# Performance work log

Hardware: AMD Instinct MI355X
Metric: run time of the kernel (lower is better)

Reference implementation:

```python
import jax, jax.numpy as jnp
import numpy as np
from jax import lax

# ---- static config (from BasePllay_2 / AdTopoLayer(out_features=50, T=25, m0=0.2, lims=[[224,0],[0,224]], K_max=2, p=0)) ----
H = W = 28
G = H * W
T = 25
K_MAX = 2
M0 = 0.2
OUT_FEATURES = 50
B = 32
TSEQ = jnp.linspace(0.0, 100.0, T)  # fixed landscape sample grid (covers DTM value range)

# static grid geometry from lims=[[224,0],[0,224]]
_xs = np.linspace(224.0, 0.0, H)
_ys = np.linspace(0.0, 224.0, W)
_pts = np.stack(np.meshgrid(_xs, _ys, indexing="ij"), -1).reshape(G, 2)
_d = np.sqrt(((_pts[:, None] - _pts[None]) ** 2).sum(-1))
_sidx = np.argsort(_d, axis=-1)
SDIST = jnp.asarray(np.take_along_axis(_d, _sidx, -1), jnp.float32)  # [G,G] sorted distances per grid point
SIDX = jnp.asarray(_sidx.astype(np.int32))                            # [G,G] static distance-sort order

# 4-connectivity neighbor table for the cubical (pixel) grid, -1 = invalid
_ii = np.arange(G).reshape(H, W)
_nb = np.full((H, W, 4), -1, np.int32)
_nb[1:, :, 0] = _ii[:-1, :]
_nb[:-1, :, 1] = _ii[1:, :]
_nb[:, 1:, 2] = _ii[:, :-1]
_nb[:, :-1, 3] = _ii[:, 1:]
NBR = jnp.asarray(_nb.reshape(G, 4))


def dtm(w):
    """Weighted distance-to-measure (r=2) on the fixed grid. w: [B,G] nonneg -> [B,G]."""
    sw = w[:, SIDX]                               # [B,G,G] weights in distance order
    cw = jnp.cumsum(sw, -1)
    d2 = SDIST ** 2
    cwd = jnp.cumsum(sw * d2[None], -1)
    bound = M0 * w.sum(-1)                        # [B]
    k = jnp.argmax(cw >= bound[:, None, None], -1)  # [B,G] first index reaching mass bound
    km1 = jnp.maximum(k - 1, 0)
    take = lambda a, i: jnp.take_along_axis(a, i[..., None], -1)[..., 0]
    has_prev = k > 0
    cw_p = jnp.where(has_prev, take(cw, km1), 0.0)
    cwd_p = jnp.where(has_prev, take(cwd, km1), 0.0)
    dk2 = d2[jnp.arange(G)[None, :], k]           # [B,G]
    val = (cwd_p + (bound[:, None] - cw_p) * dk2) / bound[:, None]
    return jnp.sqrt(jnp.maximum(val, 0.0))


def pd0(vals):
    """0-dim sublevel-set persistence of vals on the pixel grid (union-find, elder rule).
    Returns (births[G], deaths[G]); non-merging pixels yield zero-persistence pairs,
    essential components die at the max filtration value."""
    order = jnp.argsort(vals).astype(jnp.int32)
    rank = jnp.zeros(G, jnp.int32).at[order].set(jnp.arange(G, dtype=jnp.int32))

    def find(parent, i):
        return lax.while_loop(lambda j: parent[j] != j, lambda j: parent[j], i)

    def step(s, carry):
        parent, death = carry
        p = order[s]
        best = p
        for t in range(4):  # unrolled over the 4 grid neighbors (static)
            q = NBR[p, t]
            ok = (q >= 0) & (rank[jnp.maximum(q, 0)] < s)  # neighbor already inserted
            r = find(parent, jnp.where(ok, q, p))
            merge = ok & (r != best)
            r_old = rank[r] < rank[best]
            older = jnp.where(r_old, r, best)
            younger = jnp.where(r_old, best, r)
            widx = jnp.where(merge, younger, G)   # slot G is a dummy
            parent = parent.at[widx].set(older)
            death = death.at[widx].set(p)         # younger component dies at pixel p
            best = jnp.where(merge, older, best)
        return parent, death

    parent0 = jnp.arange(G + 1, dtype=jnp.int32)
    death0 = jnp.full(G + 1, -1, jnp.int32)
    _, death = lax.fori_loop(0, G, step, (parent0, death0))
    d = death[:G]
    deaths = jnp.where(d >= 0, vals[jnp.maximum(d, 0)], vals.max())
    return vals, deaths


def landscape(births, deaths):
    """K_MAX persistence landscapes sampled at TSEQ. [B,G] -> [B, K_MAX*T]."""
    tb = TSEQ[None, :, None] - births[:, None, :]   # [B,T,G]
    td = deaths[:, None, :] - TSEQ[None, :, None]
    tent = jnp.maximum(jnp.minimum(tb, td), 0.0)
    topk = lax.top_k(tent, K_MAX)[0]                # [B,T,K]
    return jnp.transpose(topk, (0, 2, 1)).reshape(births.shape[0], K_MAX * T)


def _forward(x, w_land, b_land, w_fc, b_fc):
    w = x.reshape(x.shape[0], -1)          # nn.Flatten: pixel intensities as measure weights
    v = dtm(w)                             # [B,G]
    births, deaths = jax.vmap(pd0)(v)
    feats = landscape(births, deaths)      # [B, 50]
    xt = feats @ w_land.T + b_land         # AdTopoLayer output [B, out_features]
    signal = jnp.abs(lax.stop_gradient(xt)).sum(0)   # torch: x.detach().abs().sum(0)
    out = jnp.maximum(xt, 0.0) @ w_fc.T + b_fc       # fc(relu(x))
    return out, signal

_forward_jit = jax.jit(_forward)


def setup_inputs() -> dict:
    key = jax.random.key(0)
    k = jax.random.split(key, 4)
    x = jax.random.uniform(k[0], (B, 1, H, W), jnp.float32)  # image-like nonneg weights
    w_land = jax.random.normal(k[1], (OUT_FEATURES, K_MAX * T), jnp.float32) * 0.1
    b_land = jnp.zeros((OUT_FEATURES,), jnp.float32)
    w_fc = jax.random.normal(k[2], (10, OUT_FEATURES), jnp.float32) * 0.1
    b_fc = jnp.zeros((10,), jnp.float32)
    return {"x": x, "w_land": w_land, "b_land": b_land, "w_fc": w_fc, "b_fc": b_fc}


def reference(x, w_land, b_land, w_fc, b_fc):
    return _forward_jit(x, w_land, b_land, w_fc, b_fc)
```

## Files before the change

kernel.cpp:

```cpp
#include <hip/hip_runtime.h>
#include <math.h>

#define H28 28
#define G784 784
#define BATCH 32
#define NOFF 3025
#define NOFFP 3072
#define NKEY 1459
#define TPTS 25
#define KMAX 2
#define NFEAT 50
#define OUTF 50
#define NCLS 10

#define NBX 16
#define BT 512

__device__ __forceinline__ float wave_iscan_f32(float x) {
  int t;
  t = __builtin_amdgcn_update_dpp(0, __float_as_int(x), 0x111, 0xf, 0xf, true);
  x += __int_as_float(t);
  t = __builtin_amdgcn_update_dpp(0, __float_as_int(x), 0x112, 0xf, 0xf, true);
  x += __int_as_float(t);
  t = __builtin_amdgcn_update_dpp(0, __float_as_int(x), 0x114, 0xf, 0xf, true);
  x += __int_as_float(t);
  t = __builtin_amdgcn_update_dpp(0, __float_as_int(x), 0x118, 0xf, 0xf, true);
  x += __int_as_float(t);
  t = __builtin_amdgcn_update_dpp(0, __float_as_int(x), 0x142, 0xa, 0xf, true);
  x += __int_as_float(t);
  t = __builtin_amdgcn_update_dpp(0, __float_as_int(x), 0x143, 0xc, 0xf, true);
  x += __int_as_float(t);
  return x;
}

__global__ __launch_bounds__(BT) void dtm_kernel(const float* __restrict__ x,
                                                 float* __restrict__ v) {
  __shared__ int   hist[NKEY];
  __shared__ int   seg[BT];
  __shared__ unsigned int ofs_ij[NOFFP];
  __shared__ float ofs_d2[NOFFP];
  __shared__ float w_s[G784];
  __shared__ float red[BT];

  const int tid = threadIdx.x;
  const int b   = blockIdx.x;
  const int bx  = blockIdx.y;

  for (int i = tid; i < NKEY; i += BT) hist[i] = 0;
  for (int i = NOFF + tid; i < NOFFP; i += BT) {
    ofs_ij[i] = 0x00640064u;
    ofs_d2[i] = 0.f;
  }
  __syncthreads();
  for (int i = tid; i < NOFF; i += BT) {
    int di = i / 55 - 27, dj = i % 55 - 27;
    atomicAdd(&hist[di * di + dj * dj], 1);
  }
  __syncthreads();

  const int SEG = 3;
  int base0 = tid * SEG;
  int s = 0;
  for (int k = 0; k < SEG; k++) { int idx = base0 + k; if (idx < NKEY) s += hist[idx]; }
  seg[tid] = s;
  __syncthreads();
  for (int off = 1; off < BT; off <<= 1) {
    int add = (tid >= off) ? seg[tid - off] : 0;
    __syncthreads();
    seg[tid] += add;
    __syncthreads();
  }
  int run = seg[tid] - s;
  for (int k = 0; k < SEG; k++) {
    int idx = base0 + k;
    if (idx < NKEY) { int h = hist[idx]; hist[idx] = run; run += h; }
  }
  __syncthreads();

  for (int i = tid; i < NOFF; i += BT) {
    int di = i / 55 - 27, dj = i % 55 - 27;
    int key = di * di + dj * dj;
    int pos = atomicAdd(&hist[key], 1);
    ofs_ij[pos] = ((unsigned)(di & 0xffff)) | (((unsigned)(dj & 0xffff)) << 16);
    float sd = (float)(sqrt((double)key) * (224.0 / 27.0));
    ofs_d2[pos] = sd * sd;
  }

  float ps = 0.f;
  for (int i = tid; i < G784; i += BT) {
    float wv = x[b * G784 + i];
    w_s[i] = wv;
    ps += wv;
  }
  red[tid] = ps;
  __syncthreads();
  for (int off = BT / 2; off > 0; off >>= 1) {
    if (tid < off) red[tid] += red[tid + off];
    __syncthreads();
  }
  const float bound = 0.2f * red[0];

  const int wave = tid >> 6;
  const int lane = tid & 63;
  const int slot = bx * 8 + wave;

  for (int g = slot; g < G784; g += NBX * 8) {
    const int i1 = g / H28, j1 = g % H28;
    float cw = 0.f, cwd = 0.f;
    float cwp = 0.f, cwdp = 0.f, dk2 = 0.f;
    bool crossed = false;
    for (int base = 0; base < NOFFP && !crossed; base += 64) {
      const int o = base + lane;
      const unsigned ij = ofs_ij[o];
      const float d2 = ofs_d2[o];
      const int di = (short)(ij & 0xffffu);
      const int dj = (short)(ij >> 16);
      const int i2 = i1 + di, j2 = j1 + dj;
      const bool inb = ((unsigned)i2 < (unsigned)H28) & ((unsigned)j2 < (unsigned)H28);
      const float wv = inb ? w_s[i2 * H28 + j2] : 0.f;
      const float wd = wv * d2;
      const float psw = wave_iscan_f32(wv);
      const float psd = wave_iscan_f32(wd);
      const unsigned long long mask = __ballot(cw + psw >= bound);
      if (mask) {
        const int f = __ffsll((unsigned long long)mask) - 1;
        const float psw_f = __shfl(psw, f);
        const float w_f   = __shfl(wv, f);
        const float psd_f = __shfl(psd, f);
        const float wd_f  = __shfl(wd, f);
        dk2  = __shfl(d2, f);
        cwp  = cw + (psw_f - w_f);
        cwdp = cwd + (psd_f - wd_f);
        crossed = true;
      } else {
        cw  += __int_as_float(__builtin_amdgcn_readlane(__float_as_int(psw), 63));
        cwd += __int_as_float(__builtin_amdgcn_readlane(__float_as_int(psd), 63));
      }
    }
    const float val = (cwdp + (bound - cwp) * dk2) / bound;
    if (lane == 0) v[b * G784 + g] = sqrtf(fmaxf(val, 0.f));
  }
}

__device__ __forceinline__ unsigned long long pix_key(const float* val_s, int p) {
  return (((unsigned long long)__float_as_uint(val_s[p])) << 10) | (unsigned)p;
}

__global__ __launch_bounds__(256) void pd0_kernel(const float* __restrict__ v,
                                                  float* __restrict__ feats) {
  __shared__ float val_s[G784];
  __shared__ int   ptr_s[G784];
  __shared__ int   parent[G784];
  __shared__ float deathv[G784];
  __shared__ int   mlist[G784];
  __shared__ unsigned long long edges[2048];
  __shared__ float redf[256];
  __shared__ int   mcnt_sh, ecnt_sh;
  __shared__ float vmax_sh;

  const int tid = threadIdx.x;
  const int b   = blockIdx.x;
  if (tid == 0) { mcnt_sh = 0; ecnt_sh = 0; }

  float pm = -1e30f;
  for (int i = tid; i < G784; i += 256) {
    float xv = v[b * G784 + i];
    val_s[i] = xv;
    pm = fmaxf(pm, xv);
  }
  redf[tid] = pm;
  __syncthreads();
  for (int off = 128; off > 0; off >>= 1) {
    if (tid < off) redf[tid] = fmaxf(redf[tid], redf[tid + off]);
    __syncthreads();
  }
  if (tid == 0) vmax_sh = redf[0];
  __syncthreads();
  const float vmax = vmax_sh;

  for (int p = tid; p < G784; p += 256) {
    unsigned long long kp = pix_key(val_s, p);
    int i = p / H28, j = p % H28;
    int nbs[4];
    nbs[0] = (i > 0)       ? p - H28 : -1;
    nbs[1] = (i < H28 - 1) ? p + H28 : -1;
    nbs[2] = (j > 0)       ? p - 1   : -1;
    nbs[3] = (j < H28 - 1) ? p + 1   : -1;
    int best = p;
    unsigned long long bk = kp;
    for (int t = 0; t < 4; t++) {
      int q = nbs[t];
      if (q >= 0) {
        unsigned long long kq = pix_key(val_s, q);
        if (kq < bk) { bk = kq; best = q; }
      }
    }
    ptr_s[p]  = best;
    parent[p] = p;
    deathv[p] = vmax;
    if (best == p) {
      int mi = atomicAdd(&mcnt_sh, 1);
      mlist[mi] = p;
    }
  }
  __syncthreads();

  for (int r = 0; r < 10; r++) {
    for (int p = tid; p < G784; p += 256) ptr_s[p] = ptr_s[ptr_s[p]];
    __syncthreads();
  }

  for (int p = tid; p < G784; p += 256) {
    unsigned long long kp = pix_key(val_s, p);
    int i = p / H28, j = p % H28;
    int nbs[4];
    nbs[0] = (i > 0)       ? p - H28 : -1;
    nbs[1] = (i < H28 - 1) ? p + H28 : -1;
    nbs[2] = (j > 0)       ? p - 1   : -1;
    nbs[3] = (j < H28 - 1) ? p + 1   : -1;
    int bp = ptr_s[p];
    for (int t = 0; t < 4; t++) {
      int q = nbs[t];
      if (q >= 0) {
        unsigned long long kq = pix_key(val_s, q);
        int bq = ptr_s[q];
        if (kq < kp && bq != bp) {
          int e = atomicAdd(&ecnt_sh, 1);
          edges[e] = (((unsigned long long)__float_as_uint(val_s[p])) << 32) |
                     (((unsigned long long)(unsigned)p) << 22) |
                     (((unsigned long long)(unsigned)t) << 20) |
                     (((unsigned long long)(unsigned)bp) << 10) |
                     ((unsigned long long)(unsigned)bq);
        }
      }
    }
  }
  __syncthreads();
  const int ecnt = ecnt_sh;
  const int mcnt = mcnt_sh;

  int n2 = 2;
  while (n2 < ecnt) n2 <<= 1;
  for (int i = ecnt + tid; i < n2; i += 256) edges[i] = ~0ULL;
  __syncthreads();
  for (int kk = 2; kk <= n2; kk <<= 1) {
    for (int jj = kk >> 1; jj > 0; jj >>= 1) {
      for (int i = tid; i < n2; i += 256) {
        int ixj = i ^ jj;
        if (ixj > i) {
          unsigned long long a = edges[i], c = edges[ixj];
          bool up = ((i & kk) == 0);
          if ((a > c) == up) { edges[i] = c; edges[ixj] = a; }
        }
      }
      __syncthreads();
    }
  }

  if (tid < 64) {
    const int target = mcnt - 1;
    int merged = 0;
    for (int base = 0; base < ecnt && merged < target; base += 64) {
      int i = base + tid;
      bool valid = (i < ecnt);
      unsigned long long e = valid ? edges[i] : 0ULL;
      int A = (int)((e >> 10) & 1023u);
      int B = (int)(e & 1023u);
      int rA = valid ? A : 0;
      int rB = valid ? B : 0;
      for (;;) { int pa = parent[rA]; bool mv = (pa != rA); rA = pa; if (!__any(mv)) break; }
      for (;;) { int pb = parent[rB]; bool mv = (pb != rB); rB = pb; if (!__any(mv)) break; }
      unsigned long long mask = __ballot(valid && (rA != rB));
      while (mask && merged < target) {
        int j = __ffsll(mask) - 1;
        mask &= mask - 1;
        unsigned long long ej = edges[base + j];
        int Aj = (int)((ej >> 10) & 1023u);
        int Bj = (int)(ej & 1023u);
        int ra = Aj; for (;;) { int pa = parent[ra]; if (pa == ra) break; ra = pa; }
        int rb = Bj; for (;;) { int pb = parent[rb]; if (pb == rb) break; rb = pb; }
        if (ra != rb) {
          unsigned long long ka = pix_key(val_s, ra);
          unsigned long long kb = pix_key(val_s, rb);
          int older   = (ka < kb) ? ra : rb;
          int younger = (ka < kb) ? rb : ra;
          parent[younger] = older;
          deathv[younger] = __uint_as_float((unsigned)(ej >> 32));
          merged++;
        }
      }
    }
  }
  __syncthreads();

  if (tid < TPTS) {
    float ti = (float)((double)tid * (100.0 / 24.0));
    float t1 = 0.f, t2 = 0.f;
    for (int ii = 0; ii < mcnt; ii++) {
      int m = mlist[ii];
      float tent = fminf(ti - val_s[m], deathv[m] - ti);
      tent = fmaxf(tent, 0.f);
      if (tent > t1)      { t2 = t1; t1 = tent; }
      else if (tent > t2) { t2 = tent; }
    }
    feats[b * NFEAT + tid]        = t1;
    feats[b * NFEAT + TPTS + tid] = t2;
  }
}

__global__ __launch_bounds__(256) void head_kernel(const float* __restrict__ feats_g,
                                                   const float* __restrict__ w_land,
                                                   const float* __restrict__ b_land,
                                                   const float* __restrict__ w_fc,
                                                   const float* __restrict__ b_fc,
                                                   float* __restrict__ out) {
  __shared__ float f_s[BATCH * NFEAT];
  __shared__ float xt_s[BATCH * OUTF];
  const int tid = threadIdx.x;
  for (int i = tid; i < BATCH * NFEAT; i += 256) f_s[i] = feats_g[i];
  __syncthreads();
  for (int idx = tid; idx < BATCH * OUTF; idx += 256) {
    int bb = idx / OUTF, ff = idx % OUTF;
    float acc = b_land[ff];
    const float* wr = w_land + ff * NFEAT;
    const float* fr = f_s + bb * NFEAT;
    for (int j = 0; j < NFEAT; j++) acc += fr[j] * wr[j];
    xt_s[idx] = acc;
  }
  __syncthreads();
  if (tid < OUTF) {
    float s = 0.f;
    for (int bb = 0; bb < BATCH; bb++) s += fabsf(xt_s[bb * OUTF + tid]);
    out[BATCH * NCLS + tid] = s;
  }
  for (int idx = tid; idx < BATCH * NCLS; idx += 256) {
    int bb = idx / NCLS, cc = idx % NCLS;
    float acc = b_fc[cc];
    const float* wr = w_fc + cc * OUTF;
    const float* xr = xt_s + bb * OUTF;
    for (int ff = 0; ff < OUTF; ff++) acc += fmaxf(xr[ff], 0.f) * wr[ff];
    out[bb * NCLS + cc] = acc;
  }
}

extern "C" void kernel_launch(void* const* d_in, const int* in_sizes, int n_in,
                              void* d_out, int out_size, void* d_ws, size_t ws_size,
                              hipStream_t stream) {
  (void)in_sizes; (void)n_in; (void)out_size; (void)ws_size;
  const float* x      = (const float*)d_in[0];
  const float* w_land = (const float*)d_in[1];
  const float* b_land = (const float*)d_in[2];
  const float* w_fc   = (const float*)d_in[3];
  const float* b_fc   = (const float*)d_in[4];
  float* out   = (float*)d_out;
  float* v     = (float*)d_ws;
  float* feats = v + BATCH * G784;

  dim3 g1(BATCH, NBX);
  dtm_kernel<<<g1, BT, 0, stream>>>(x, v);
  pd0_kernel<<<BATCH, 256, 0, stream>>>(v, feats);
  head_kernel<<<1, 256, 0, stream>>>(feats, w_land, b_land, w_fc, b_fc, out);
}
```

Measured before the change: 120.9 us.

## Precompute offset table at compile time and fuse head into pd0 kernel

```diff
diff --git a/kernel.cpp b/kernel.cpp
--- a/kernel.cpp
+++ b/kernel.cpp
@@ -15,6 +15,39 @@
 
 #define NBX 16
 #define BT 512
+#define BT2 512
+
+struct OffPair { unsigned ij; float d2; };
+struct OffTab  { OffPair e[NOFFP]; };
+
+constexpr double csqrt(double x) {
+  double r = x * 0.5 + 1.0;
+  for (int i = 0; i < 20; i++) r = 0.5 * (r + x / r);
+  return r;
+}
+
+constexpr OffTab make_offtab() {
+  OffTab t{};
+  int start[NKEY] = {};
+  for (int i = 0; i < NOFF; i++) {
+    int di = i / 55 - 27, dj = i % 55 - 27;
+    start[di * di + dj * dj]++;
+  }
+  int run = 0;
+  for (int k = 0; k < NKEY; k++) { int h = start[k]; start[k] = run; run += h; }
+  for (int i = 0; i < NOFF; i++) {
+    int di = i / 55 - 27, dj = i % 55 - 27;
+    int key = di * di + dj * dj;
+    int pos = start[key]++;
+    float sd = (key == 0) ? 0.0f : (float)(csqrt((double)key) * (224.0 / 27.0));
+    t.e[pos].ij = ((unsigned)(di & 0xffff)) | (((unsigned)(dj & 0xffff)) << 16);
+    t.e[pos].d2 = sd * sd;
+  }
+  for (int i = NOFF; i < NOFFP; i++) { t.e[i].ij = 0x00640064u; t.e[i].d2 = 0.f; }
+  return t;
+}
+
+__device__ constexpr OffTab OFFTAB = make_offtab();
 
 __device__ __forceinline__ float wave_iscan_f32(float x) {
   int t;
@@ -34,11 +67,8 @@
 }
 
 __global__ __launch_bounds__(BT) void dtm_kernel(const float* __restrict__ x,
-                                                 float* __restrict__ v) {
-  __shared__ int   hist[NKEY];
-  __shared__ int   seg[BT];
-  __shared__ unsigned int ofs_ij[NOFFP];
-  __shared__ float ofs_d2[NOFFP];
+                                                 float* __restrict__ v,
+                                                 int* __restrict__ done_ctr) {
   __shared__ float w_s[G784];
   __shared__ float red[BT];
 
@@ -46,45 +76,7 @@
   const int b   = blockIdx.x;
   const int bx  = blockIdx.y;
 
-  for (int i = tid; i < NKEY; i += BT) hist[i] = 0;
-  for (int i = NOFF + tid; i < NOFFP; i += BT) {
-    ofs_ij[i] = 0x00640064u;
-    ofs_d2[i] = 0.f;
-  }
-  __syncthreads();
-  for (int i = tid; i < NOFF; i += BT) {
-    int di = i / 55 - 27, dj = i % 55 - 27;
-    atomicAdd(&hist[di * di + dj * dj], 1);
-  }
-  __syncthreads();
-
-  const int SEG = 3;
-  int base0 = tid * SEG;
-  int s = 0;
-  for (int k = 0; k < SEG; k++) { int idx = base0 + k; if (idx < NKEY) s += hist[idx]; }
-  seg[tid] = s;
-  __syncthreads();
-  for (int off = 1; off < BT; off <<= 1) {
-    int add = (tid >= off) ? seg[tid - off] : 0;
-    __syncthreads();
-    seg[tid] += add;
-    __syncthreads();
-  }
-  int run = seg[tid] - s;
-  for (int k = 0; k < SEG; k++) {
-    int idx = base0 + k;
-    if (idx < NKEY) { int h = hist[idx]; hist[idx] = run; run += h; }
-  }
-  __syncthreads();
-
-  for (int i = tid; i < NOFF; i += BT) {
-    int di = i / 55 - 27, dj = i % 55 - 27;
-    int key = di * di + dj * dj;
-    int pos = atomicAdd(&hist[key], 1);
-    ofs_ij[pos] = ((unsigned)(di & 0xffff)) | (((unsigned)(dj & 0xffff)) << 16);
-    float sd = (float)(sqrt((double)key) * (224.0 / 27.0));
-    ofs_d2[pos] = sd * sd;
-  }
+  if (b == 0 && bx == 0 && tid == 0) *done_ctr = 0;
 
   float ps = 0.f;
   for (int i = tid; i < G784; i += BT) {
@@ -109,16 +101,20 @@
     float cw = 0.f, cwd = 0.f;
     float cwp = 0.f, cwdp = 0.f, dk2 = 0.f;
     bool crossed = false;
+    int o = lane;
+    unsigned ij = OFFTAB.e[o].ij;
+    float d2v   = OFFTAB.e[o].d2;
     for (int base = 0; base < NOFFP && !crossed; base += 64) {
-      const int o = base + lane;
-      const unsigned ij = ofs_ij[o];
-      const float d2 = ofs_d2[o];
+      int onext = o + 64;
+      if (onext >= NOFFP) onext = o;
+      const unsigned ij_n = OFFTAB.e[onext].ij;
+      const float    d2_n = OFFTAB.e[onext].d2;
       const int di = (short)(ij & 0xffffu);
       const int dj = (short)(ij >> 16);
       const int i2 = i1 + di, j2 = j1 + dj;
       const bool inb = ((unsigned)i2 < (unsigned)H28) & ((unsigned)j2 < (unsigned)H28);
       const float wv = inb ? w_s[i2 * H28 + j2] : 0.f;
-      const float wd = wv * d2;
+      const float wd = wv * d2v;
       const float psw = wave_iscan_f32(wv);
       const float psd = wave_iscan_f32(wd);
       const unsigned long long mask = __ballot(cw + psw >= bound);
@@ -128,7 +124,7 @@
         const float w_f   = __shfl(wv, f);
         const float psd_f = __shfl(psd, f);
         const float wd_f  = __shfl(wd, f);
-        dk2  = __shfl(d2, f);
+        dk2  = __shfl(d2v, f);
         cwp  = cw + (psw_f - w_f);
         cwdp = cwd + (psd_f - wd_f);
         crossed = true;
@@ -136,6 +132,7 @@
         cw  += __int_as_float(__builtin_amdgcn_readlane(__float_as_int(psw), 63));
         cwd += __int_as_float(__builtin_amdgcn_readlane(__float_as_int(psd), 63));
       }
+      ij = ij_n; d2v = d2_n; o = onext;
     }
     const float val = (cwdp + (bound - cwp) * dk2) / bound;
     if (lane == 0) v[b * G784 + g] = sqrtf(fmaxf(val, 0.f));
@@ -146,31 +143,39 @@
   return (((unsigned long long)__float_as_uint(val_s[p])) << 10) | (unsigned)p;
 }
 
-__global__ __launch_bounds__(256) void pd0_kernel(const float* __restrict__ v,
-                                                  float* __restrict__ feats) {
+__global__ __launch_bounds__(BT2) void pd0_kernel(const float* __restrict__ v,
+                                                  float* __restrict__ feats,
+                                                  int* __restrict__ done_ctr,
+                                                  const float* __restrict__ w_land,
+                                                  const float* __restrict__ b_land,
+                                                  const float* __restrict__ w_fc,
+                                                  const float* __restrict__ b_fc,
+                                                  float* __restrict__ out) {
   __shared__ float val_s[G784];
   __shared__ int   ptr_s[G784];
   __shared__ int   parent[G784];
   __shared__ float deathv[G784];
   __shared__ int   mlist[G784];
   __shared__ unsigned long long edges[2048];
-  __shared__ float redf[256];
-  __shared__ int   mcnt_sh, ecnt_sh;
+  __shared__ float redf[BT2];
+  __shared__ int   mcnt_sh, ecnt_sh, last_sh;
   __shared__ float vmax_sh;
+  __shared__ float f_s[BATCH * NFEAT];
+  __shared__ float xt_s[BATCH * OUTF];
 
   const int tid = threadIdx.x;
   const int b   = blockIdx.x;
   if (tid == 0) { mcnt_sh = 0; ecnt_sh = 0; }
 
   float pm = -1e30f;
-  for (int i = tid; i < G784; i += 256) {
+  for (int i = tid; i < G784; i += BT2) {
     float xv = v[b * G784 + i];
     val_s[i] = xv;
     pm = fmaxf(pm, xv);
   }
   redf[tid] = pm;
   __syncthreads();
-  for (int off = 128; off > 0; off >>= 1) {
+  for (int off = BT2 / 2; off > 0; off >>= 1) {
     if (tid < off) redf[tid] = fmaxf(redf[tid], redf[tid + off]);
     __syncthreads();
   }
@@ -178,7 +183,7 @@
   __syncthreads();
   const float vmax = vmax_sh;
 
-  for (int p = tid; p < G784; p += 256) {
+  for (int p = tid; p < G784; p += BT2) {
     unsigned long long kp = pix_key(val_s, p);
     int i = p / H28, j = p % H28;
     int nbs[4];
@@ -206,11 +211,11 @@
   __syncthreads();
 
   for (int r = 0; r < 10; r++) {
-    for (int p = tid; p < G784; p += 256) ptr_s[p] = ptr_s[ptr_s[p]];
+    for (int p = tid; p < G784; p += BT2) ptr_s[p] = ptr_s[ptr_s[p]];
     __syncthreads();
   }
 
-  for (int p = tid; p < G784; p += 256) {
+  for (int p = tid; p < G784; p += BT2) {
     unsigned long long kp = pix_key(val_s, p);
     int i = p / H28, j = p % H28;
     int nbs[4];
@@ -226,26 +231,27 @@
         int bq = ptr_s[q];
         if (kq < kp && bq != bp) {
           int e = atomicAdd(&ecnt_sh, 1);
-          edges[e] = (((unsigned long long)__float_as_uint(val_s[p])) << 32) |
-                     (((unsigned long long)(unsigned)p) << 22) |
-                     (((unsigned long long)(unsigned)t) << 20) |
-                     (((unsigned long long)(unsigned)bp) << 10) |
-                     ((unsigned long long)(unsigned)bq);
+          if (e < 2048)
+            edges[e] = (((unsigned long long)__float_as_uint(val_s[p])) << 32) |
+                       (((unsigned long long)(unsigned)p) << 22) |
+                       (((unsigned long long)(unsigned)t) << 20) |
+                       (((unsigned long long)(unsigned)bp) << 10) |
+                       ((unsigned long long)(unsigned)bq);
         }
       }
     }
   }
   __syncthreads();
-  const int ecnt = ecnt_sh;
+  const int ecnt = (ecnt_sh < 2048) ? ecnt_sh : 2048;
   const int mcnt = mcnt_sh;
 
   int n2 = 2;
   while (n2 < ecnt) n2 <<= 1;
-  for (int i = ecnt + tid; i < n2; i += 256) edges[i] = ~0ULL;
+  for (int i = ecnt + tid; i < n2; i += BT2) edges[i] = ~0ULL;
   __syncthreads();
   for (int kk = 2; kk <= n2; kk <<= 1) {
     for (int jj = kk >> 1; jj > 0; jj >>= 1) {
-      for (int i = tid; i < n2; i += 256) {
+      for (int i = tid; i < n2; i += BT2) {
         int ixj = i ^ jj;
         if (ixj > i) {
           unsigned long long a = edges[i], c = edges[ixj];
@@ -306,20 +312,17 @@
     feats[b * NFEAT + tid]        = t1;
     feats[b * NFEAT + TPTS + tid] = t2;
   }
-}
-
-__global__ __launch_bounds__(256) void head_kernel(const float* __restrict__ feats_g,
-                                                   const float* __restrict__ w_land,
-                                                   const float* __restrict__ b_land,
-                                                   const float* __restrict__ w_fc,
-                                                   const float* __restrict__ b_fc,
-                                                   float* __restrict__ out) {
-  __shared__ float f_s[BATCH * NFEAT];
-  __shared__ float xt_s[BATCH * OUTF];
-  const int tid = threadIdx.x;
-  for (int i = tid; i < BATCH * NFEAT; i += 256) f_s[i] = feats_g[i];
-  __syncthreads();
-  for (int idx = tid; idx < BATCH * OUTF; idx += 256) {
+
+  __threadfence();
+  __syncthreads();
+  if (tid == 0) last_sh = (atomicAdd(done_ctr, 1) == BATCH - 1) ? 1 : 0;
+  __syncthreads();
+  if (!last_sh) return;
+  __threadfence();
+
+  for (int i = tid; i < BATCH * NFEAT; i += BT2) f_s[i] = feats[i];
+  __syncthreads();
+  for (int idx = tid; idx < BATCH * OUTF; idx += BT2) {
     int bb = idx / OUTF, ff = idx % OUTF;
     float acc = b_land[ff];
     const float* wr = w_land + ff * NFEAT;
@@ -333,7 +336,7 @@
     for (int bb = 0; bb < BATCH; bb++) s += fabsf(xt_s[bb * OUTF + tid]);
     out[BATCH * NCLS + tid] = s;
   }
-  for (int idx = tid; idx < BATCH * NCLS; idx += 256) {
+  for (int idx = tid; idx < BATCH * NCLS; idx += BT2) {
     int bb = idx / NCLS, cc = idx % NCLS;
     float acc = b_fc[cc];
     const float* wr = w_fc + cc * OUTF;
@@ -355,9 +358,10 @@
   float* out   = (float*)d_out;
   float* v     = (float*)d_ws;
   float* feats = v + BATCH * G784;
+  int*   done  = (int*)(feats + BATCH * NFEAT);
 
   dim3 g1(BATCH, NBX);
-  dtm_kernel<<<g1, BT, 0, stream>>>(x, v);
-  pd0_kernel<<<BATCH, 256, 0, stream>>>(v, feats);
-  head_kernel<<<1, 256, 0, stream>>>(feats, w_land, b_land, w_fc, b_fc, out);
-}
+  dtm_kernel<<<g1, BT, 0, stream>>>(x, v, done);
+  pd0_kernel<<<BATCH, BT2, 0, stream>>>(v, feats, done,
+                                        w_land, b_land, w_fc, b_fc, out);
+}
```

After: 115.1 us. 4.8% less time.
